# Kernel optimization log

Measured on AMD Instinct MI355X. Metric: run time of the kernel, lower is better.

Reference implementation:

```python
import jax, jax.numpy as jnp
import numpy as np

E = 320000   # edges
N = 10000    # nodes (len(set(idx_i)))
F = 128      # feature dim f
NRBF = 20    # n
R_CUT = 5.0


def setup_inputs() -> dict:
    key = jax.random.key(0)
    ks = jax.random.split(key, 8)
    s = jax.random.normal(ks[0], (E, 1, F), dtype=jnp.float32)
    r = jax.random.normal(ks[1], (E, 3), dtype=jnp.float32)
    v = jax.random.normal(ks[2], (E, 3, F), dtype=jnp.float32)
    idx_i = jax.random.randint(ks[3], (E,), 0, N)
    # phi layer: Linear(F -> 3F), internal_w_layer: Linear(NRBF -> 3F)
    W_phi = jax.random.normal(ks[4], (F, 3 * F), dtype=jnp.float32) * 0.02
    b_phi = jnp.zeros((3 * F,), dtype=jnp.float32)
    W_w = jax.random.normal(ks[5], (NRBF, 3 * F), dtype=jnp.float32) * 0.02
    b_w = jnp.zeros((3 * F,), dtype=jnp.float32)
    return {"s": s, "r": r, "v": v, "idx_i": idx_i,
            "W_phi": W_phi, "b_phi": b_phi, "W_w": W_w, "b_w": b_w}


def reference(s, r, v, idx_i, W_phi, b_phi, W_w, b_w):
    # phi(s): [E,1,3F]
    phi_out = s @ W_phi + b_phi
    org_r = jax.lax.stop_gradient(r)            # r.detach().clone()
    # RBF: sin(n*pi/r_cut * |r|) / |r|  -> [E,1,NRBF]
    r_norm = jnp.linalg.norm(r, axis=1, keepdims=True)[..., None]   # [E,1,1]
    n_vals = jnp.arange(1, NRBF + 1, dtype=s.dtype)                 # [NRBF]
    rbf = jnp.sin(n_vals * (jnp.pi / R_CUT) * r_norm) / r_norm      # [E,1,NRBF]
    # cosine cutoff applied to rbf values (faithful to the source)
    rbf = jnp.where(rbf <= R_CUT, 0.5 * (jnp.cos(jnp.pi * rbf / R_CUT) + 1.0), 0.0)
    w = rbf @ W_w + b_w                          # [E,1,3F]
    split = w * phi_out                          # [E,1,3F]
    sv, ss, sr = split[..., :F], split[..., F:2 * F], split[..., 2 * F:]
    # scalar messages: scatter-add ss into nodes -> [N,1,F]
    out_s = jax.ops.segment_sum(ss, idx_i, num_segments=N)
    # vector messages
    org_rn = org_r / jnp.linalg.norm(org_r)      # global Frobenius norm (faithful)
    vr = sr * org_rn[:, :, None]                 # [E,3,F]
    v_msg = sv * v + vr                          # [E,3,F]
    out_v = jax.ops.segment_sum(v_msg, idx_i, num_segments=N)  # [N,3,F]
    return (out_v, out_s)
```

## Files before the change

### kernel.cpp

```cpp
#include <hip/hip_runtime.h>

#define E_EDGES 320000
#define N_NODES 10000
#define F_DIM   128
#define C_DIM   384
#define NRBF_K  20
#define TILE    16
#define TP      20
#define PI_F    3.14159265358979323846f

__global__ void sumsq_kernel(const float* __restrict__ r,
                             float* __restrict__ out) {
    __shared__ float red[4];
    int tid = blockIdx.x * blockDim.x + threadIdx.x;
    int stride = gridDim.x * blockDim.x;
    float acc = 0.f;
    for (int i = tid; i < E_EDGES * 3; i += stride) {
        float x = r[i];
        acc += x * x;
    }
    #pragma unroll
    for (int off = 32; off > 0; off >>= 1)
        acc += __shfl_down(acc, off, 64);
    int lane = threadIdx.x & 63;
    int wave = threadIdx.x >> 6;
    if (lane == 0) red[wave] = acc;
    __syncthreads();
    if (threadIdx.x == 0) {
        float s = red[0] + red[1] + red[2] + red[3];
        atomicAdd(out, s);
    }
}

__global__ __launch_bounds__(384) void main_kernel(
    const float* __restrict__ s,
    const float* __restrict__ r,
    const float* __restrict__ v,
    const int*   __restrict__ idx_i,
    const float* __restrict__ W_phi,
    const float* __restrict__ b_phi,
    const float* __restrict__ W_w,
    const float* __restrict__ b_w,
    const float* __restrict__ sumsq,
    float* __restrict__ out_v,
    float* __restrict__ out_s)
{
    __shared__ float s_tile[F_DIM][TP];
    __shared__ float rbf_sh[NRBF_K][TP];
    __shared__ float orn_sh[TILE][3];
    __shared__ float split_sh[C_DIM][TILE + 1];
    __shared__ int   idx_sh[TILE];

    const int tid = threadIdx.x;
    const int j   = tid;
    const float inv_gn = rsqrtf(*sumsq);
    const float bp = b_phi[j];
    const float bw = b_w[j];

    const int ntiles = E_EDGES / TILE;
    for (int t = blockIdx.x; t < ntiles; t += gridDim.x) {
        const int e0 = t * TILE;

        for (int q = tid; q < TILE * F_DIM; q += 384) {
            int e = q >> 7, k = q & 127;
            s_tile[k][e] = s[(size_t)(e0 + e) * F_DIM + k];
        }
        if (tid < TILE * NRBF_K) {
            int e = tid / NRBF_K, n = tid % NRBF_K;
            float r0 = r[(e0 + e) * 3 + 0];
            float r1 = r[(e0 + e) * 3 + 1];
            float r2 = r[(e0 + e) * 3 + 2];
            float rn = sqrtf(r0 * r0 + r1 * r1 + r2 * r2);
            float arg  = (float)(n + 1) * (PI_F / 5.0f) * rn;
            float tval = sinf(arg) / rn;
            float env  = (tval <= 5.0f) ? 0.5f * (cosf(PI_F * tval / 5.0f) + 1.0f)
                                        : 0.0f;
            rbf_sh[n][e] = env;
        }
        if (tid >= 320 && tid < 320 + TILE * 3) {
            int q = tid - 320; int e = q / 3, d = q % 3;
            orn_sh[e][d] = r[(e0 + e) * 3 + d] * inv_gn;
        }
        if (tid >= 368) {
            idx_sh[tid - 368] = idx_i[e0 + (tid - 368)];
        }
        __syncthreads();

        float accp[TILE], accw[TILE];
        #pragma unroll
        for (int e = 0; e < TILE; e++) { accp[e] = bp; accw[e] = bw; }

        for (int k = 0; k < F_DIM; k++) {
            float wv = W_phi[k * C_DIM + j];
            const float4* s4 = (const float4*)(&s_tile[k][0]);
            float sv[TILE];
            *(float4*)&sv[0]  = s4[0];
            *(float4*)&sv[4]  = s4[1];
            *(float4*)&sv[8]  = s4[2];
            *(float4*)&sv[12] = s4[3];
            #pragma unroll
            for (int e = 0; e < TILE; e++) accp[e] += wv * sv[e];
        }
        #pragma unroll
        for (int n = 0; n < NRBF_K; n++) {
            float wv = W_w[n * C_DIM + j];
            const float4* r4 = (const float4*)(&rbf_sh[n][0]);
            float rv[TILE];
            *(float4*)&rv[0]  = r4[0];
            *(float4*)&rv[4]  = r4[1];
            *(float4*)&rv[8]  = r4[2];
            *(float4*)&rv[12] = r4[3];
            #pragma unroll
            for (int e = 0; e < TILE; e++) accw[e] += wv * rv[e];
        }
        #pragma unroll
        for (int e = 0; e < TILE; e++) split_sh[j][e] = accp[e] * accw[e];
        __syncthreads();

        const int f = tid & 127;
        const int d = tid >> 7;
        for (int e = 0; e < TILE; e++) {
            int   idx = idx_sh[e];
            float svv = split_sh[f][e];
            float srr = split_sh[256 + f][e];
            float vv  = v[(size_t)(e0 + e) * C_DIM + tid];
            float msg = svv * vv + srr * orn_sh[e][d];
            atomicAdd(&out_v[((size_t)idx * 3 + d) * F_DIM + f], msg);
            if (d == 0) {
                float ss = split_sh[128 + f][e];
                atomicAdd(&out_s[(size_t)idx * F_DIM + f], ss);
            }
        }
        __syncthreads();
    }
}

extern "C" void kernel_launch(void* const* d_in, const int* in_sizes, int n_in,
                              void* d_out, int out_size, void* d_ws, size_t ws_size,
                              hipStream_t stream) {
    const float* s     = (const float*)d_in[0];
    const float* r     = (const float*)d_in[1];
    const float* v     = (const float*)d_in[2];
    const int*   idx_i = (const int*)d_in[3];
    const float* W_phi = (const float*)d_in[4];
    const float* b_phi = (const float*)d_in[5];
    const float* W_w   = (const float*)d_in[6];
    const float* b_w   = (const float*)d_in[7];

    float* out   = (float*)d_out;
    float* sumsq = (float*)d_ws;
    const int NV = N_NODES * 3 * F_DIM;

    hipMemsetAsync(d_out, 0, (size_t)out_size * sizeof(float), stream);
    hipMemsetAsync(d_ws, 0, 16, stream);
    sumsq_kernel<<<512, 256, 0, stream>>>(r, sumsq);
    main_kernel<<<1024, 384, 0, stream>>>(s, r, v, idx_i, W_phi, b_phi, W_w, b_w,
                                          sumsq, out, out + NV);
}
```

Before: 2.110 ms.

## Replace atomic scatter with CSR sort-by-node and per-node gather reduction

Builds a CSR index over destination nodes with histogram, scan and fill kernels, then launches one block per node that gathers that node's edges, computes the messages and sums them in registers. This removes the per-element global atomics into out_v and out_s and the output memset. The cost is three extra small kernels, gathered (non-contiguous) reads of s, r and v, and padded partial tiles, since nodes average about 32 edges. Edge order within a node is nondeterministic because of the atomic fill.

```diff
diff --git a/kernel.cpp b/kernel.cpp
--- a/kernel.cpp
+++ b/kernel.cpp
@@ -9,8 +9,12 @@
 #define TP      20
 #define PI_F    3.14159265358979323846f
 
-__global__ void sumsq_kernel(const float* __restrict__ r,
-                             float* __restrict__ out) {
+#define WS_CNT_OFF   16
+#define WS_ROW_OFF   40016
+#define WS_CUR_OFF   80020
+#define WS_ORD_OFF   120020
+
+__global__ void sumsq_kernel(const float* __restrict__ r, float* __restrict__ out) {
     __shared__ float red[4];
     int tid = blockIdx.x * blockDim.x + threadIdx.x;
     int stride = gridDim.x * blockDim.x;
@@ -26,69 +30,117 @@
     int wave = threadIdx.x >> 6;
     if (lane == 0) red[wave] = acc;
     __syncthreads();
-    if (threadIdx.x == 0) {
-        float s = red[0] + red[1] + red[2] + red[3];
-        atomicAdd(out, s);
-    }
-}
-
-__global__ __launch_bounds__(384) void main_kernel(
+    if (threadIdx.x == 0) atomicAdd(out, red[0] + red[1] + red[2] + red[3]);
+}
+
+__global__ void hist_kernel(const int* __restrict__ idx_i, int* __restrict__ cnt) {
+    int e = blockIdx.x * blockDim.x + threadIdx.x;
+    if (e < E_EDGES) atomicAdd(&cnt[idx_i[e]], 1);
+}
+
+__global__ __launch_bounds__(1024) void scan_kernel(const int* __restrict__ cnt,
+                                                    int* __restrict__ row,
+                                                    int* __restrict__ cur) {
+    __shared__ int sdata[1024];
+    __shared__ int carry;
+    const int tid = threadIdx.x;
+    if (tid == 0) carry = 0;
+    __syncthreads();
+    for (int base = 0; base < N_NODES; base += 1024) {
+        int x = (base + tid < N_NODES) ? cnt[base + tid] : 0;
+        sdata[tid] = x;
+        __syncthreads();
+        #pragma unroll
+        for (int off = 1; off < 1024; off <<= 1) {
+            int y = (tid >= off) ? sdata[tid - off] : 0;
+            __syncthreads();
+            sdata[tid] += y;
+            __syncthreads();
+        }
+        int excl = carry + sdata[tid] - x;
+        if (base + tid < N_NODES) { row[base + tid] = excl; cur[base + tid] = excl; }
+        __syncthreads();
+        if (tid == 0) carry += sdata[1023];
+        __syncthreads();
+    }
+    if (tid == 0) row[N_NODES] = E_EDGES;
+}
+
+__global__ void fill_kernel(const int* __restrict__ idx_i,
+                            int* __restrict__ cur, int* __restrict__ order) {
+    int e = blockIdx.x * blockDim.x + threadIdx.x;
+    if (e < E_EDGES) {
+        int pos = atomicAdd(&cur[idx_i[e]], 1);
+        order[pos] = e;
+    }
+}
+
+__global__ __launch_bounds__(384) void gather_kernel(
     const float* __restrict__ s,
     const float* __restrict__ r,
     const float* __restrict__ v,
-    const int*   __restrict__ idx_i,
     const float* __restrict__ W_phi,
     const float* __restrict__ b_phi,
     const float* __restrict__ W_w,
     const float* __restrict__ b_w,
     const float* __restrict__ sumsq,
-    float* __restrict__ out_v,
-    float* __restrict__ out_s)
+    const int*   __restrict__ row,
+    const int*   __restrict__ order,
+    float* __restrict__ out)
 {
     __shared__ float s_tile[F_DIM][TP];
     __shared__ float rbf_sh[NRBF_K][TP];
     __shared__ float orn_sh[TILE][3];
     __shared__ float split_sh[C_DIM][TILE + 1];
-    __shared__ int   idx_sh[TILE];
+    __shared__ int   eid_sh[TILE];
 
     const int tid = threadIdx.x;
     const int j   = tid;
+    const int n   = blockIdx.x;
+    const int beg = row[n];
+    const int cnt = row[n + 1] - beg;
     const float inv_gn = rsqrtf(*sumsq);
     const float bp = b_phi[j];
     const float bw = b_w[j];
-
-    const int ntiles = E_EDGES / TILE;
-    for (int t = blockIdx.x; t < ntiles; t += gridDim.x) {
-        const int e0 = t * TILE;
+    const int f = tid & 127;
+    const int d = tid >> 7;
+
+    float acc_v = 0.f, acc_s = 0.f;
+
+    for (int base = 0; base < cnt; base += TILE) {
+        const int m = min(TILE, cnt - base);
 
         for (int q = tid; q < TILE * F_DIM; q += 384) {
-            int e = q >> 7, k = q & 127;
-            s_tile[k][e] = s[(size_t)(e0 + e) * F_DIM + k];
+            int sl = q >> 7, k = q & 127;
+            int eid = order[beg + base + min(sl, m - 1)];
+            s_tile[k][sl] = s[(size_t)eid * F_DIM + k];
         }
         if (tid < TILE * NRBF_K) {
-            int e = tid / NRBF_K, n = tid % NRBF_K;
-            float r0 = r[(e0 + e) * 3 + 0];
-            float r1 = r[(e0 + e) * 3 + 1];
-            float r2 = r[(e0 + e) * 3 + 2];
+            int sl = tid / NRBF_K, nb = tid % NRBF_K;
+            int eid = order[beg + base + min(sl, m - 1)];
+            float r0 = r[eid * 3 + 0];
+            float r1 = r[eid * 3 + 1];
+            float r2 = r[eid * 3 + 2];
             float rn = sqrtf(r0 * r0 + r1 * r1 + r2 * r2);
-            float arg  = (float)(n + 1) * (PI_F / 5.0f) * rn;
+            float arg  = (float)(nb + 1) * (PI_F / 5.0f) * rn;
             float tval = sinf(arg) / rn;
-            float env  = (tval <= 5.0f) ? 0.5f * (cosf(PI_F * tval / 5.0f) + 1.0f)
-                                        : 0.0f;
-            rbf_sh[n][e] = env;
+            rbf_sh[nb][sl] = (tval <= 5.0f) ? 0.5f * (cosf(PI_F * tval / 5.0f) + 1.0f)
+                                            : 0.0f;
         }
         if (tid >= 320 && tid < 320 + TILE * 3) {
-            int q = tid - 320; int e = q / 3, d = q % 3;
-            orn_sh[e][d] = r[(e0 + e) * 3 + d] * inv_gn;
+            int q = tid - 320; int sl = q / 3, dd = q % 3;
+            int eid = order[beg + base + min(sl, m - 1)];
+            orn_sh[sl][dd] = r[eid * 3 + dd] * inv_gn;
         }
         if (tid >= 368) {
-            idx_sh[tid - 368] = idx_i[e0 + (tid - 368)];
+            int sl = tid - 368;
+            eid_sh[sl] = order[beg + base + min(sl, m - 1)];
         }
         __syncthreads();
 
         float accp[TILE], accw[TILE];
         #pragma unroll
-        for (int e = 0; e < TILE; e++) { accp[e] = bp; accw[e] = bw; }
+        for (int sl = 0; sl < TILE; sl++) { accp[sl] = bp; accw[sl] = bw; }
 
         for (int k = 0; k < F_DIM; k++) {
             float wv = W_phi[k * C_DIM + j];
@@ -99,40 +151,35 @@
             *(float4*)&sv[8]  = s4[2];
             *(float4*)&sv[12] = s4[3];
             #pragma unroll
-            for (int e = 0; e < TILE; e++) accp[e] += wv * sv[e];
-        }
-        #pragma unroll
-        for (int n = 0; n < NRBF_K; n++) {
-            float wv = W_w[n * C_DIM + j];
-            const float4* r4 = (const float4*)(&rbf_sh[n][0]);
+            for (int sl = 0; sl < TILE; sl++) accp[sl] += wv * sv[sl];
+        }
+        #pragma unroll
+        for (int nb = 0; nb < NRBF_K; nb++) {
+            float wv = W_w[nb * C_DIM + j];
+            const float4* r4 = (const float4*)(&rbf_sh[nb][0]);
             float rv[TILE];
             *(float4*)&rv[0]  = r4[0];
             *(float4*)&rv[4]  = r4[1];
             *(float4*)&rv[8]  = r4[2];
             *(float4*)&rv[12] = r4[3];
             #pragma unroll
-            for (int e = 0; e < TILE; e++) accw[e] += wv * rv[e];
-        }
-        #pragma unroll
-        for (int e = 0; e < TILE; e++) split_sh[j][e] = accp[e] * accw[e];
-        __syncthreads();
-
-        const int f = tid & 127;
-        const int d = tid >> 7;
-        for (int e = 0; e < TILE; e++) {
-            int   idx = idx_sh[e];
-            float svv = split_sh[f][e];
-            float srr = split_sh[256 + f][e];
-            float vv  = v[(size_t)(e0 + e) * C_DIM + tid];
-            float msg = svv * vv + srr * orn_sh[e][d];
-            atomicAdd(&out_v[((size_t)idx * 3 + d) * F_DIM + f], msg);
-            if (d == 0) {
-                float ss = split_sh[128 + f][e];
-                atomicAdd(&out_s[(size_t)idx * F_DIM + f], ss);
-            }
-        }
-        __syncthreads();
-    }
+            for (int sl = 0; sl < TILE; sl++) accw[sl] += wv * rv[sl];
+        }
+        #pragma unroll
+        for (int sl = 0; sl < TILE; sl++) split_sh[j][sl] = accp[sl] * accw[sl];
+        __syncthreads();
+
+        for (int sl = 0; sl < m; sl++) {
+            int eid = eid_sh[sl];
+            float vv  = v[(size_t)eid * C_DIM + tid];
+            acc_v += split_sh[f][sl] * vv + split_sh[256 + f][sl] * orn_sh[sl][d];
+            if (d == 0) acc_s += split_sh[128 + f][sl];
+        }
+        __syncthreads();
+    }
+
+    out[(size_t)n * C_DIM + tid] = acc_v;
+    if (d == 0) out[(size_t)N_NODES * C_DIM + n * F_DIM + f] = acc_s;
 }
 
 extern "C" void kernel_launch(void* const* d_in, const int* in_sizes, int n_in,
@@ -148,12 +195,19 @@
     const float* b_w   = (const float*)d_in[7];
 
     float* out   = (float*)d_out;
-    float* sumsq = (float*)d_ws;
-    const int NV = N_NODES * 3 * F_DIM;
-
-    hipMemsetAsync(d_out, 0, (size_t)out_size * sizeof(float), stream);
-    hipMemsetAsync(d_ws, 0, 16, stream);
+    char*  ws    = (char*)d_ws;
+    float* sumsq = (float*)ws;
+    int*   cnt   = (int*)(ws + WS_CNT_OFF);
+    int*   rowp  = (int*)(ws + WS_ROW_OFF);
+    int*   cur   = (int*)(ws + WS_CUR_OFF);
+    int*   order = (int*)(ws + WS_ORD_OFF);
+
+    hipMemsetAsync(d_ws, 0, WS_CNT_OFF + N_NODES * sizeof(int), stream);
+
     sumsq_kernel<<<512, 256, 0, stream>>>(r, sumsq);
-    main_kernel<<<1024, 384, 0, stream>>>(s, r, v, idx_i, W_phi, b_phi, W_w, b_w,
-                                          sumsq, out, out + NV);
-}
+    hist_kernel<<<(E_EDGES + 255) / 256, 256, 0, stream>>>(idx_i, cnt);
+    scan_kernel<<<1, 1024, 0, stream>>>(cnt, rowp, cur);
+    fill_kernel<<<(E_EDGES + 255) / 256, 256, 0, stream>>>(idx_i, cur, order);
+    gather_kernel<<<N_NODES, 384, 0, stream>>>(s, r, v, W_phi, b_phi, W_w, b_w,
+                                               sumsq, rowp, order, out);
+}
```

After: 2.350 ms. +11.4%, slower.
